# Kernel tuning notes

Measured on AMD Instinct MI355X. Metric: run time of the kernel, lower is better.

## Reference

```python
import jax, jax.numpy as jnp
import numpy as np

IN_C = 64
OUT_C = 128
HEADS = 8
DIM = 9 * IN_C  # 576


def unfold3x3_s2(fea):
    # torch.nn.functional.unfold(fea, (3,3), padding=1, stride=2)
    # returns [N, C*9, L] with channel-major (c, kh, kw) ordering.
    N, C, H, W = fea.shape
    Ho, Wo = H // 2, W // 2
    p = jnp.pad(fea, ((0, 0), (0, 0), (1, 1), (1, 1)))
    patches = jnp.stack(
        [p[:, :, ki:ki + 2 * Ho:2, kj:kj + 2 * Wo:2] for ki in range(3) for kj in range(3)],
        axis=2,
    )  # [N, C, 9, Ho, Wo]
    return patches.reshape(N, C * 9, Ho * Wo)


def mhsa(x, w_qkv, b_qkv, w_out, b_out):
    # standard ViT attention: x [B, L, D]
    B, L, D = x.shape
    dh = D // HEADS
    qkv = x @ w_qkv + b_qkv  # [B, L, 3D]
    q, k, v = jnp.split(qkv, 3, axis=-1)
    def heads(t):
        return t.reshape(B, L, HEADS, dh).transpose(0, 2, 1, 3)  # [B, h, L, dh]
    q, k, v = heads(q), heads(k), heads(v)
    scale = dh ** -0.5
    scores = jnp.einsum('bhqd,bhkd->bhqk', q, k) * scale
    attn = jax.nn.softmax(scores, axis=-1)
    o = jnp.einsum('bhqk,bhkd->bhqd', attn, v)  # [B, h, L, dh]
    o = o.transpose(0, 2, 1, 3).reshape(B, L, D)
    return o @ w_out + b_out


def setup_inputs() -> dict:
    key = jax.random.key(0)
    ks = jax.random.split(key, 6)
    s = DIM ** -0.5
    return {
        'fea': jax.random.normal(ks[0], (1, IN_C, 128, 128), dtype=jnp.float32),
        'w_qkv': jax.random.normal(ks[1], (DIM, 3 * DIM), dtype=jnp.float32) * s,
        'b_qkv': jnp.zeros((3 * DIM,), dtype=jnp.float32),
        'w_out': jax.random.normal(ks[2], (DIM, DIM), dtype=jnp.float32) * s,
        'b_out': jnp.zeros((DIM,), dtype=jnp.float32),
        'conv_w': jax.random.normal(ks[3], (OUT_C, IN_C, 3, 3), dtype=jnp.float32) * s,
    }


def reference(fea, w_qkv, b_qkv, w_out, b_out, conv_w):
    N, C, H, W = fea.shape
    Ho, Wo = H // 2, W // 2
    x = unfold3x3_s2(fea).transpose(0, 2, 1)          # [N, L, 9C]
    x = mhsa(x, w_qkv, b_qkv, w_out, b_out) + x       # residual
    # matmul with reshaped conv weights: [N, L, 9C] @ [9C, out_c]
    y = x @ conv_w.reshape(OUT_C, -1).T               # [N, L, out_c]
    y = y.transpose(0, 2, 1).reshape(N, OUT_C, Ho, Wo)  # fold with (1,1) kernel
    return jax.nn.silu(y)
```

## Files before the change

### kernel.cpp

```cpp
#include <hip/hip_runtime.h>
#include <hip/hip_bf16.h>
#include <math.h>

#define L_TOK 4096
#define D_DIM 576
#define NHEADS 8
#define DHEAD 72
#define DPAD 96
#define HSZ ((size_t)NHEADS * L_TOK * DPAD)
#define KSPLIT 4
#define LOG2E 1.4426950408889634f
#define SCALE2 (0.11785113019775792f * 1.4426950408889634f)

typedef __attribute__((ext_vector_type(8))) short short8;
typedef __attribute__((ext_vector_type(4))) short short4v;
typedef __attribute__((ext_vector_type(4))) float float4v;

union F4S8 {
  float4 f4;
  short8 s8;
  __hip_bfloat16 h[8];
};

__device__ inline void tc_body(const float* __restrict__ src,
                               __hip_bfloat16* __restrict__ dst, int R, int C,
                               int bi, int bj, int t, __hip_bfloat16* Ts) {
  const int col = t & 63, row4 = t >> 6;
#pragma unroll
  for (int u = 0; u < 16; u++) {
    int r = u * 4 + row4;
    Ts[r * 68 + col] = __float2bfloat16(src[(size_t)(bj * 64 + r) * C + bi * 64 + col]);
  }
  __syncthreads();
#pragma unroll
  for (int u = 0; u < 16; u++) {
    int c = u * 4 + row4;
    dst[(size_t)(bi * 64 + c) * R + bj * 64 + col] = Ts[col * 68 + c];
  }
}

__global__ __launch_bounds__(256) void prep_all(const float* __restrict__ fea,
                                                const float* __restrict__ w_qkv,
                                                const float* __restrict__ w_out,
                                                const float* __restrict__ conv_w,
                                                __hip_bfloat16* __restrict__ xb,
                                                __hip_bfloat16* __restrict__ WqkvT,
                                                __hip_bfloat16* __restrict__ WoT,
                                                __hip_bfloat16* __restrict__ CwB) {
  __shared__ float Shm[3120];
  const int b = blockIdx.x;
  const int t = threadIdx.x;
  if (b < 512) {
    float* Lf = Shm;
    const int ho = b & 63;
    const int c0 = (b >> 6) * 8;
    for (int e = t; e < 3072; e += 256) {
      int c = e / 384;
      int rr = (e / 128) % 3;
      int w = e & 127;
      int h = 2 * ho + rr - 1;
      float v = 0.f;
      if ((unsigned)h < 128u) v = fea[(size_t)(c0 + c) * 16384 + h * 128 + w];
      Lf[(c * 3 + rr) * 130 + w + 1] = v;
    }
    if (t < 24) { Lf[t * 130] = 0.f; Lf[t * 130 + 129] = 0.f; }
    __syncthreads();
    for (int e = t; e < 576; e += 256) {
      int wo = e / 9, ch = e - wo * 9;
      F4S8 u;
#pragma unroll
      for (int j = 0; j < 8; j++) {
        int dd = ch * 8 + j;
        int c = dd / 9, k = dd - c * 9;
        int ki = k / 3, kj = k - ki * 3;
        u.h[j] = __float2bfloat16(Lf[(c * 3 + ki) * 130 + 2 * wo + kj]);
      }
      *(float4*)(xb + (size_t)(ho * 64 + wo) * D_DIM + c0 * 9 + ch * 8) = u.f4;
    }
  } else if (b < 755) {
    int bb = b - 512;
    tc_body(w_qkv, WqkvT, D_DIM, 1728, bb % 27, bb / 27, t, (__hip_bfloat16*)Shm);
  } else if (b < 836) {
    int bb = b - 755;
    tc_body(w_out, WoT, D_DIM, D_DIM, bb % 9, bb / 9, t, (__hip_bfloat16*)Shm);
  } else {
    int i = (b - 836) * 256 + t;
    CwB[i] = __float2bfloat16(conv_w[i]);
  }
}

template <int EPI, int NMI>
__global__ __launch_bounds__(256) void gemm_mfma(const __hip_bfloat16* __restrict__ A,
                                                 const __hip_bfloat16* __restrict__ Bt,
                                                 const float* __restrict__ bias,
                                                 const __hip_bfloat16* __restrict__ resid,
                                                 __hip_bfloat16* __restrict__ outB,
                                                 __hip_bfloat16* __restrict__ outB2) {
  constexpr int K = D_DIM;
  constexpr int BM = NMI * 32;
  __shared__ __align__(16) __hip_bfloat16 As[BM * 72];
  __shared__ __align__(16) __hip_bfloat16 Bs[64 * 72];
  const int t = threadIdx.x;
  const int wave = t >> 6, lane = t & 63, quad = lane >> 4, l16 = lane & 15;
  const int wm = (wave & 2) * (NMI * 8);
  const int wn = (wave & 1) * 32;
  const int m0 = blockIdx.x * BM, n0 = blockIdx.y * 64;

  float4v acc[NMI][2];
#pragma unroll
  for (int i = 0; i < NMI; i++)
#pragma unroll
    for (int j = 0; j < 2; j++) acc[i][j] = (float4v){0.f, 0.f, 0.f, 0.f};

  const int arow = t >> 3, ach = t & 7;
  for (int k0 = 0; k0 < K; k0 += 64) {
    __syncthreads();
#pragma unroll
    for (int u = 0; u < NMI; u++) {
      int row = u * 32 + arow;
      *(float4*)(&As[row * 72 + ach * 8]) =
          *(const float4*)(A + (size_t)(m0 + row) * K + k0 + ach * 8);
    }
#pragma unroll
    for (int u = 0; u < 2; u++) {
      int row = u * 32 + arow;
      *(float4*)(&Bs[row * 72 + ach * 8]) =
          *(const float4*)(Bt + (size_t)(n0 + row) * K + k0 + ach * 8);
    }
    __syncthreads();
    short8 af[NMI][2], bfr[2][2];
#pragma unroll
    for (int i = 0; i < NMI; i++)
#pragma unroll
      for (int s = 0; s < 2; s++)
        af[i][s] = *(const short8*)(&As[(wm + i * 16 + l16) * 72 + s * 32 + quad * 8]);
#pragma unroll
    for (int j = 0; j < 2; j++)
#pragma unroll
      for (int s = 0; s < 2; s++)
        bfr[j][s] = *(const short8*)(&Bs[(wn + j * 16 + l16) * 72 + s * 32 + quad * 8]);
#pragma unroll
    for (int i = 0; i < NMI; i++)
#pragma unroll
      for (int j = 0; j < 2; j++) {
        acc[i][j] = __builtin_amdgcn_mfma_f32_16x16x32_bf16(af[i][0], bfr[j][0], acc[i][j], 0, 0, 0);
        acc[i][j] = __builtin_amdgcn_mfma_f32_16x16x32_bf16(af[i][1], bfr[j][1], acc[i][j], 0, 0, 0);
      }
  }

  if (EPI == 0) {
    const int part = n0 / D_DIM;
    if (part < 2) {
      __hip_bfloat16* dst = outB + (size_t)part * HSZ;
      const float sc = (part == 0) ? SCALE2 : 1.f;
#pragma unroll
      for (int j = 0; j < 2; j++) {
        int ng = n0 + wn + j * 16 + l16;
        float bv = bias[ng];
        int rem = ng - part * D_DIM;
        int h = rem / DHEAD;
        int d = rem - h * DHEAD;
#pragma unroll
        for (int i = 0; i < NMI; i++) {
          int mb = m0 + wm + i * 16 + quad * 4;
#pragma unroll
          for (int r = 0; r < 4; r++)
            dst[((size_t)h * L_TOK + mb + r) * DPAD + d] =
                __float2bfloat16((acc[i][j][r] + bv) * sc);
        }
      }
    } else {
      __hip_bfloat16* Ls = As;
      __syncthreads();
      const int n0rel = n0 - 2 * D_DIM;
#pragma unroll
      for (int j = 0; j < 2; j++) {
        int nloc = wn + j * 16 + l16;
        float bv = bias[n0 + nloc];
#pragma unroll
        for (int i = 0; i < NMI; i++) {
          int mloc = wm + i * 16 + quad * 4;
#pragma unroll
          for (int r = 0; r < 4; r++)
            Ls[nloc * 136 + mloc + r] = __float2bfloat16(acc[i][j][r] + bv);
        }
      }
      __syncthreads();
      for (int e = t; e < 1024; e += 256) {
        int row = e >> 4, ch = e & 15;
        int ng = n0rel + row;
        int hh = ng / DHEAD, dd = ng - hh * DHEAD;
        *(float4*)(outB2 + ((size_t)hh * DPAD + dd) * L_TOK + m0 + ch * 8) =
            *(const float4*)(&Ls[row * 136 + ch * 8]);
      }
    }
  } else {
#pragma unroll
    for (int j = 0; j < 2; j++) {
      int ng = n0 + wn + j * 16 + l16;
      float bv = bias[ng];
#pragma unroll
      for (int i = 0; i < NMI; i++) {
        int mb = m0 + wm + i * 16 + quad * 4;
#pragma unroll
        for (int r = 0; r < 4; r++) {
          size_t idx = (size_t)(mb + r) * D_DIM + ng;
          float v = acc[i][j][r] + bv + __bfloat162float(resid[idx]);
          outB[idx] = __float2bfloat16(v);
        }
      }
    }
  }
}

__global__ __launch_bounds__(256) void final_small(const __hip_bfloat16* __restrict__ A,
                                                   const __hip_bfloat16* __restrict__ Bt,
                                                   float* __restrict__ out) {
  __shared__ __align__(16) __hip_bfloat16 As[32 * 72];
  __shared__ __align__(16) __hip_bfloat16 Bs[32 * 72];
  const int t = threadIdx.x;
  const int wave = t >> 6, lane = t & 63, quad = lane >> 4, l16 = lane & 15;
  const int wm = (wave & 2) * 8;
  const int wn = (wave & 1) * 16;
  const int m0 = blockIdx.x * 32, n0 = blockIdx.y * 32;

  float4v acc = (float4v){0.f, 0.f, 0.f, 0.f};

  const int arow = t >> 3, ach = t & 7;
  for (int k0 = 0; k0 < D_DIM; k0 += 64) {
    __syncthreads();
    *(float4*)(&As[arow * 72 + ach * 8]) =
        *(const float4*)(A + (size_t)(m0 + arow) * D_DIM + k0 + ach * 8);
    *(float4*)(&Bs[arow * 72 + ach * 8]) =
        *(const float4*)(Bt + (size_t)(n0 + arow) * D_DIM + k0 + ach * 8);
    __syncthreads();
    short8 af[2], bfr[2];
#pragma unroll
    for (int s = 0; s < 2; s++) {
      af[s] = *(const short8*)(&As[(wm + l16) * 72 + s * 32 + quad * 8]);
      bfr[s] = *(const short8*)(&Bs[(wn + l16) * 72 + s * 32 + quad * 8]);
    }
    acc = __builtin_amdgcn_mfma_f32_16x16x32_bf16(af[0], bfr[0], acc, 0, 0, 0);
    acc = __builtin_amdgcn_mfma_f32_16x16x32_bf16(af[1], bfr[1], acc, 0, 0, 0);
  }
  const int oc = n0 + wn + l16;
  const int mb = m0 + wm + quad * 4;
#pragma unroll
  for (int r = 0; r < 4; r++) {
    float v = acc[r];
    float sg = 1.f / (1.f + __expf(-v));
    out[(size_t)oc * L_TOK + mb + r] = v * sg;
  }
}

#define KS_STRIDE 88
#define VT_STRIDE 72
#define PS_STRIDE 40
#define KBUF (64 * KS_STRIDE)
#define VBUF (74 * VT_STRIDE)

__global__ __launch_bounds__(256, 3) void attn_mfma(const __hip_bfloat16* __restrict__ Qb,
                                                    const __hip_bfloat16* __restrict__ Kb,
                                                    const __hip_bfloat16* __restrict__ VbT,
                                                    __hip_bfloat16* __restrict__ Opart,
                                                    float* __restrict__ Ml) {
  __shared__ __align__(16) __hip_bfloat16 Ks[2 * KBUF];
  __shared__ __align__(16) __hip_bfloat16 Vt[2 * VBUF];
  __shared__ __align__(16) __hip_bfloat16 Ps[4 * 32 * PS_STRIDE];

  const int bid = blockIdx.x;
  const int h = bid & 7;
  const int rest = bid >> 3;
  const int ksp = rest & 3;
  const int qblk = rest >> 2;
  const int t = threadIdx.x;
  const int wave = t >> 6;
  const int lane = t & 63;
  const int quad = lane >> 4;
  const int l16 = lane & 15;

  const __hip_bfloat16* Qh = Qb + (size_t)h * L_TOK * DPAD;
  const __hip_bfloat16* Kh = Kb + (size_t)h * L_TOK * DPAD;
  const __hip_bfloat16* VhT = VbT + (size_t)h * DPAD * L_TOK;

  const int qbase = qblk * 128 + wave * 32;
  short8 qf[2][3];
#pragma unroll
  for (int mi = 0; mi < 2; mi++) {
#pragma unroll
    for (int s = 0; s < 3; s++) {
      if (s == 2 && quad >= 1) {
        qf[mi][s] = (short8){0, 0, 0, 0, 0, 0, 0, 0};
        if (quad == 1) qf[mi][s][0] = (short)0xC100;
      } else {
        qf[mi][s] = *(const short8*)(Qh + (size_t)(qbase + mi * 16 + l16) * DPAD + s * 32 + quad * 8);
      }
    }
  }

  {
    const float4 zero4 = {0.f, 0.f, 0.f, 0.f};
    union { float4 f4; unsigned u[4]; } kpad, vones;
    kpad.u[0] = 0x00003F80u; kpad.u[1] = 0u; kpad.u[2] = 0u; kpad.u[3] = 0u;
    vones.u[0] = vones.u[1] = vones.u[2] = vones.u[3] = 0x3F803F80u;
    if (t < 128) {
      int row = t & 63, buf = t >> 6;
      __hip_bfloat16* B = Ks + buf * KBUF;
      *(float4*)(&B[row * KS_STRIDE + 72]) = kpad.f4;
      *(float4*)(&B[row * KS_STRIDE + 80]) = zero4;
    } else if (t < 160) {
      int e = t - 128;
      int buf = e >> 4, r2 = (e >> 3) & 1, ch = e & 7;
      __hip_bfloat16* B = Vt + buf * VBUF;
      *(float4*)(&B[(72 + r2) * VT_STRIDE + ch * 8]) = r2 ? zero4 : vones.f4;
    }
  }

  float4v Of[2][5];
#pragma unroll
  for (int mi = 0; mi < 2; mi++)
#pragma unroll
    for (int nt = 0; nt < 5; nt++) Of[mi][nt] = (float4v){0.f, 0.f, 0.f, 0.f};

  __hip_bfloat16* myPs = Ps + wave * 32 * PS_STRIDE;
  const int kstart = ksp * 1024;

  int kgo[3], klo[3], vgo[3], vlo[3];
#pragma unroll
  for (int u = 0; u < 3; u++) {
    int e = t + u * 256;
    int ee = (e < 576) ? e : 0;
    int row = ee / 9, ch = ee - row * 9;
    kgo[u] = row * (DPAD * 2) + ch * 16;
    klo[u] = row * (KS_STRIDE * 2) + ch * 16;
    int d = ee >> 3, c2 = ee & 7;
    vgo[u] = d * (L_TOK * 2) + c2 * 16;
    vlo[u] = d * (VT_STRIDE * 2) + c2 * 16;
  }
  const bool has3 = (t < 64);

  float4 krg0, krg1, krg2, vrg0, vrg1, vrg2;
  auto load_K = [&](int kbase) {
    const char* Kt_ = (const char*)(Kh + (size_t)kbase * DPAD);
    krg0 = *(const float4*)(Kt_ + kgo[0]);
    krg1 = *(const float4*)(Kt_ + kgo[1]);
    if (has3) krg2 = *(const float4*)(Kt_ + kgo[2]);
  };
  auto load_V = [&](int kbase) {
    const char* Vg_ = (const char*)(VhT + kbase);
    vrg0 = *(const float4*)(Vg_ + vgo[0]);
    vrg1 = *(const float4*)(Vg_ + vgo[1]);
    if (has3) vrg2 = *(const float4*)(Vg_ + vgo[2]);
  };
  auto stage_write = [&](__hip_bfloat16* Kw, __hip_bfloat16* Vw) {
    *(float4*)((char*)Kw + klo[0]) = krg0;
    *(float4*)((char*)Kw + klo[1]) = krg1;
    *(float4*)((char*)Vw + vlo[0]) = vrg0;
    *(float4*)((char*)Vw + vlo[1]) = vrg1;
    if (has3) {
      *(float4*)((char*)Kw + klo[2]) = krg2;
      *(float4*)((char*)Vw + vlo[2]) = vrg2;
    }
  };

  auto body = [&](int kt, const __hip_bfloat16* Ksb, const __hip_bfloat16* Vtb,
                  __hip_bfloat16* Kw, __hip_bfloat16* Vw) {
    const int knext = (kt < 15) ? kt + 1 : 15;
    load_K(kstart + knext * 64);

    float4v S[2][4];
    __builtin_amdgcn_s_setprio(1);
#pragma unroll
    for (int ks = 0; ks < 4; ks++) {
      float4v a0 = (float4v){0.f, 0.f, 0.f, 0.f};
      float4v a1 = a0;
#pragma unroll
      for (int s = 0; s < 2; s++) {
        short8 kf = *(const short8*)(&Ksb[(ks * 16 + l16) * KS_STRIDE + s * 32 + quad * 8]);
        a0 = __builtin_amdgcn_mfma_f32_16x16x32_bf16(kf, qf[0][s], a0, 0, 0, 0);
        a1 = __builtin_amdgcn_mfma_f32_16x16x32_bf16(kf, qf[1][s], a1, 0, 0, 0);
      }
      {
        int c2s = 64 + (quad < 2 ? quad * 8 : 16);
        short8 kf2 = *(const short8*)(&Ksb[(ks * 16 + l16) * KS_STRIDE + c2s]);
        a0 = __builtin_amdgcn_mfma_f32_16x16x32_bf16(kf2, qf[0][2], a0, 0, 0, 0);
        a1 = __builtin_amdgcn_mfma_f32_16x16x32_bf16(kf2, qf[1][2], a1, 0, 0, 0);
      }
#pragma unroll
      for (int r = 0; r < 4; r++) { S[0][ks][r] = a0[r]; S[1][ks][r] = a1[r]; }
    }
    __builtin_amdgcn_s_setprio(0);

    load_V(kstart + knext * 64);

#pragma unroll
    for (int kstep = 0; kstep < 2; kstep++) {
#pragma unroll
      for (int mi = 0; mi < 2; mi++) {
#pragma unroll
        for (int k2 = 0; k2 < 2; k2++) {
          int ks = kstep * 2 + k2;
          union { short4v v; __hip_bfloat16 hh[4]; } pk;
#pragma unroll
          for (int r = 0; r < 4; r++)
            pk.hh[r] = __float2bfloat16(exp2f(S[mi][ks][r]));
          *(short4v*)(&myPs[(mi * 16 + l16) * PS_STRIDE + k2 * 16 + quad * 4]) = pk.v;
        }
      }
      short8 pa[2];
#pragma unroll
      for (int mi = 0; mi < 2; mi++)
        pa[mi] = *(const short8*)(&myPs[(mi * 16 + l16) * PS_STRIDE + quad * 8]);
      __builtin_amdgcn_s_setprio(1);
#pragma unroll
      for (int nt = 0; nt < 4; nt++) {
        short8 vb = *(const short8*)(&Vtb[(nt * 16 + l16) * VT_STRIDE + kstep * 32 + quad * 8]);
        Of[0][nt] = __builtin_amdgcn_mfma_f32_16x16x32_bf16(pa[0], vb, Of[0][nt], 0, 0, 0);
        Of[1][nt] = __builtin_amdgcn_mfma_f32_16x16x32_bf16(pa[1], vb, Of[1][nt], 0, 0, 0);
      }
      {
        int vrow = 64 + l16;
        vrow = vrow > 73 ? 73 : vrow;
        short8 vb4 = *(const short8*)(&Vtb[vrow * VT_STRIDE + kstep * 32 + quad * 8]);
        Of[0][4] = __builtin_amdgcn_mfma_f32_16x16x32_bf16(pa[0], vb4, Of[0][4], 0, 0, 0);
        Of[1][4] = __builtin_amdgcn_mfma_f32_16x16x32_bf16(pa[1], vb4, Of[1][4], 0, 0, 0);
      }
      __builtin_amdgcn_s_setprio(0);
    }

    stage_write(Kw, Vw);
    __syncthreads();
  };

  load_K(kstart);
  load_V(kstart);
  stage_write(Ks, Vt);
  __syncthreads();

  for (int kt2 = 0; kt2 < 16; kt2 += 2) {
    body(kt2,     Ks,        Vt,        Ks + KBUF, Vt + VBUF);
    body(kt2 + 1, Ks + KBUF, Vt + VBUF, Ks,        Vt);
  }

  const size_t pb = ((size_t)ksp * NHEADS + h) * L_TOK;
#pragma unroll
  for (int mi = 0; mi < 2; mi++) {
#pragma unroll
    for (int nt = 0; nt < 5; nt++) {
      int d = nt * 16 + l16;
      if (d < DHEAD) {
#pragma unroll
        for (int r = 0; r < 4; r++) {
          int q = qbase + mi * 16 + quad * 4 + r;
          Opart[(pb + q) * 72 + d] = __float2bfloat16(Of[mi][nt][r]);
        }
      }
    }
  }
  if (l16 == 8) {
#pragma unroll
    for (int mi = 0; mi < 2; mi++) {
#pragma unroll
      for (int r = 0; r < 4; r++)
        Ml[pb + qbase + mi * 16 + quad * 4 + r] = Of[mi][4][r];
    }
  }
}

__global__ __launch_bounds__(256) void attn_merge(const __hip_bfloat16* __restrict__ Opart,
                                                  const float* __restrict__ Ml,
                                                  __hip_bfloat16* __restrict__ ob) {
  int idx = blockIdx.x * 256 + threadIdx.x;
  int h = idx / (L_TOK * 9);
  int rem = idx - h * (L_TOK * 9);
  int q = rem / 9;
  int ch = rem - q * 9;
  float denom = 0.f;
  float acc[8] = {0, 0, 0, 0, 0, 0, 0, 0};
#pragma unroll
  for (int s = 0; s < KSPLIT; s++) {
    size_t b = ((size_t)s * NHEADS + h) * L_TOK + q;
    denom += Ml[b];
    short8 o = *(const short8*)(Opart + b * 72 + ch * 8);
#pragma unroll
    for (int j = 0; j < 8; j++) {
      union { short ss; __hip_bfloat16 bb; } u;
      u.ss = o[j];
      acc[j] += __bfloat162float(u.bb);
    }
  }
  float inv = 1.f / denom;
  __hip_bfloat16* dst = ob + (size_t)q * D_DIM + h * DHEAD + ch * 8;
#pragma unroll
  for (int j = 0; j < 8; j++) dst[j] = __float2bfloat16(acc[j] * inv);
}

extern "C" void kernel_launch(void* const* d_in, const int* in_sizes, int n_in,
                              void* d_out, int out_size, void* d_ws, size_t ws_size,
                              hipStream_t stream) {
  const float* fea    = (const float*)d_in[0];
  const float* w_qkv  = (const float*)d_in[1];
  const float* b_qkv  = (const float*)d_in[2];
  const float* w_out  = (const float*)d_in[3];
  const float* b_out  = (const float*)d_in[4];
  const float* conv_w = (const float*)d_in[5];
  float* out = (float*)d_out;

  __hip_bfloat16* xb    = (__hip_bfloat16*)d_ws;
  __hip_bfloat16* WqkvT = xb + (size_t)L_TOK * D_DIM;
  __hip_bfloat16* WoT   = WqkvT + (size_t)1728 * D_DIM;
  __hip_bfloat16* CwB   = WoT + (size_t)D_DIM * D_DIM;
  __hip_bfloat16* QKb   = CwB + (size_t)128 * D_DIM;
  __hip_bfloat16* VbT   = QKb + 2 * HSZ;
  __hip_bfloat16* Opart = VbT + HSZ;
  float* Ml = (float*)(Opart + (size_t)KSPLIT * NHEADS * L_TOK * 72);
  __hip_bfloat16* ob = QKb;
  __hip_bfloat16* xr = Opart;

  prep_all<<<1124, 256, 0, stream>>>(fea, w_qkv, w_out, conv_w, xb, WqkvT, WoT, CwB);
  gemm_mfma<0, 4><<<dim3(32, 27), 256, 0, stream>>>(xb, WqkvT, b_qkv, nullptr, QKb, VbT);
  attn_mfma<<<1024, 256, 0, stream>>>(QKb, QKb + HSZ, VbT, Opart, Ml);
  attn_merge<<<1152, 256, 0, stream>>>(Opart, Ml, ob);
  gemm_mfma<1, 2><<<dim3(64, 9), 256, 0, stream>>>(ob, WoT, b_out, xb, xr, nullptr);
  final_small<<<dim3(128, 4), 256, 0, stream>>>(xr, CwB, out);
}
```

Measured before the change: 179.1 us.

## Stage K/V tiles with direct global-to-LDS loads and XOR-swizzled V layout

Replaces register-staged K/V tile loads (global to VGPR, then LDS store) with global_load_lds 16-byte direct copies into packed, unpadded LDS tiles. V columns are XOR-swizzled on the global side so packed rows avoid bank conflicts. The padding rows and columns now come from a small constant LDS array selected per lane. This removes register pressure and extra LDS store instructions, at the cost of relying on correct vmcnt handling across the barrier and of per-lane pointer selects for the pad fragments.

Result: faster. 173.2 us (-3.3%).

```diff
diff --git a/kernel.cpp b/kernel.cpp
--- a/kernel.cpp
+++ b/kernel.cpp
@@ -21,6 +21,12 @@
   short8 s8;
   __hip_bfloat16 h[8];
 };
+
+__device__ __forceinline__ void gl16(const void* g, void* l) {
+  __builtin_amdgcn_global_load_lds(
+      (const __attribute__((address_space(1))) unsigned int*)g,
+      (__attribute__((address_space(3))) unsigned int*)l, 16, 0, 0);
+}
 
 __device__ inline void tc_body(const float* __restrict__ src,
                                __hip_bfloat16* __restrict__ dst, int R, int C,
@@ -253,20 +259,21 @@
   }
 }
 
-#define KS_STRIDE 88
-#define VT_STRIDE 72
+#define KSE 72
+#define VSE 64
+#define KTILE (64 * KSE)
+#define VTILE (72 * VSE)
 #define PS_STRIDE 40
-#define KBUF (64 * KS_STRIDE)
-#define VBUF (74 * VT_STRIDE)
 
 __global__ __launch_bounds__(256, 3) void attn_mfma(const __hip_bfloat16* __restrict__ Qb,
                                                     const __hip_bfloat16* __restrict__ Kb,
                                                     const __hip_bfloat16* __restrict__ VbT,
                                                     __hip_bfloat16* __restrict__ Opart,
                                                     float* __restrict__ Ml) {
-  __shared__ __align__(16) __hip_bfloat16 Ks[2 * KBUF];
-  __shared__ __align__(16) __hip_bfloat16 Vt[2 * VBUF];
+  __shared__ __align__(16) __hip_bfloat16 Ks[2 * KTILE];
+  __shared__ __align__(16) __hip_bfloat16 Vt[2 * VTILE];
   __shared__ __align__(16) __hip_bfloat16 Ps[4 * 32 * PS_STRIDE];
+  __shared__ __align__(16) __hip_bfloat16 PadC[32];
 
   const int bid = blockIdx.x;
   const int h = bid & 7;
@@ -283,6 +290,14 @@
   const __hip_bfloat16* Kh = Kb + (size_t)h * L_TOK * DPAD;
   const __hip_bfloat16* VhT = VbT + (size_t)h * DPAD * L_TOK;
 
+  if (t < 4) {
+    union { float4 f4; unsigned u[4]; } pv;
+    pv.u[0] = pv.u[1] = pv.u[2] = pv.u[3] = 0u;
+    if (t == 0) pv.u[0] = 0x00003F80u;
+    if (t == 2) pv.u[0] = pv.u[1] = pv.u[2] = pv.u[3] = 0x3F803F80u;
+    *(float4*)(&PadC[t * 8]) = pv.f4;
+  }
+
   const int qbase = qblk * 128 + wave * 32;
   short8 qf[2][3];
 #pragma unroll
@@ -298,24 +313,6 @@
     }
   }
 
-  {
-    const float4 zero4 = {0.f, 0.f, 0.f, 0.f};
-    union { float4 f4; unsigned u[4]; } kpad, vones;
-    kpad.u[0] = 0x00003F80u; kpad.u[1] = 0u; kpad.u[2] = 0u; kpad.u[3] = 0u;
-    vones.u[0] = vones.u[1] = vones.u[2] = vones.u[3] = 0x3F803F80u;
-    if (t < 128) {
-      int row = t & 63, buf = t >> 6;
-      __hip_bfloat16* B = Ks + buf * KBUF;
-      *(float4*)(&B[row * KS_STRIDE + 72]) = kpad.f4;
-      *(float4*)(&B[row * KS_STRIDE + 80]) = zero4;
-    } else if (t < 160) {
-      int e = t - 128;
-      int buf = e >> 4, r2 = (e >> 3) & 1, ch = e & 7;
-      __hip_bfloat16* B = Vt + buf * VBUF;
-      *(float4*)(&B[(72 + r2) * VT_STRIDE + ch * 8]) = r2 ? zero4 : vones.f4;
-    }
-  }
-
   float4v Of[2][5];
 #pragma unroll
   for (int mi = 0; mi < 2; mi++)
@@ -325,49 +322,35 @@
   __hip_bfloat16* myPs = Ps + wave * 32 * PS_STRIDE;
   const int kstart = ksp * 1024;
 
-  int kgo[3], klo[3], vgo[3], vlo[3];
+  int kgo[3], vgo[3];
 #pragma unroll
   for (int u = 0; u < 3; u++) {
     int e = t + u * 256;
     int ee = (e < 576) ? e : 0;
     int row = ee / 9, ch = ee - row * 9;
     kgo[u] = row * (DPAD * 2) + ch * 16;
-    klo[u] = row * (KS_STRIDE * 2) + ch * 16;
     int d = ee >> 3, c2 = ee & 7;
-    vgo[u] = d * (L_TOK * 2) + c2 * 16;
-    vlo[u] = d * (VT_STRIDE * 2) + c2 * 16;
-  }
-  const bool has3 = (t < 64);
-
-  float4 krg0, krg1, krg2, vrg0, vrg1, vrg2;
-  auto load_K = [&](int kbase) {
-    const char* Kt_ = (const char*)(Kh + (size_t)kbase * DPAD);
-    krg0 = *(const float4*)(Kt_ + kgo[0]);
-    krg1 = *(const float4*)(Kt_ + kgo[1]);
-    if (has3) krg2 = *(const float4*)(Kt_ + kgo[2]);
+    vgo[u] = d * (L_TOK * 2) + ((c2 ^ (d & 7)) * 16);
+  }
+
+  auto stage = [&](int kbase, int p) {
+    const char* Kg = (const char*)(Kh + (size_t)kbase * DPAD);
+    const char* Vg = (const char*)(VhT + kbase);
+    char* Kl = (char*)Ks + p * (KTILE * 2) + t * 16;
+    char* Vl = (char*)Vt + p * (VTILE * 2) + t * 16;
+    gl16(Kg + kgo[0], Kl);
+    gl16(Kg + kgo[1], Kl + 4096);
+    gl16(Vg + vgo[0], Vl);
+    gl16(Vg + vgo[1], Vl + 4096);
+    if (wave == 0) {
+      gl16(Kg + kgo[2], Kl + 8192);
+      gl16(Vg + vgo[2], Vl + 8192);
+    }
   };
-  auto load_V = [&](int kbase) {
-    const char* Vg_ = (const char*)(VhT + kbase);
-    vrg0 = *(const float4*)(Vg_ + vgo[0]);
-    vrg1 = *(const float4*)(Vg_ + vgo[1]);
-    if (has3) vrg2 = *(const float4*)(Vg_ + vgo[2]);
-  };
-  auto stage_write = [&](__hip_bfloat16* Kw, __hip_bfloat16* Vw) {
-    *(float4*)((char*)Kw + klo[0]) = krg0;
-    *(float4*)((char*)Kw + klo[1]) = krg1;
-    *(float4*)((char*)Vw + vlo[0]) = vrg0;
-    *(float4*)((char*)Vw + vlo[1]) = vrg1;
-    if (has3) {
-      *(float4*)((char*)Kw + klo[2]) = krg2;
-      *(float4*)((char*)Vw + vlo[2]) = vrg2;
-    }
-  };
-
-  auto body = [&](int kt, const __hip_bfloat16* Ksb, const __hip_bfloat16* Vtb,
-                  __hip_bfloat16* Kw, __hip_bfloat16* Vw) {
-    const int knext = (kt < 15) ? kt + 1 : 15;
-    load_K(kstart + knext * 64);
-
+
+  const int vswz = l16 & 7;
+
+  auto compute = [&](const __hip_bfloat16* Ksb, const __hip_bfloat16* Vtb) {
     float4v S[2][4];
     __builtin_amdgcn_s_setprio(1);
 #pragma unroll
@@ -376,13 +359,15 @@
       float4v a1 = a0;
 #pragma unroll
       for (int s = 0; s < 2; s++) {
-        short8 kf = *(const short8*)(&Ksb[(ks * 16 + l16) * KS_STRIDE + s * 32 + quad * 8]);
+        short8 kf = *(const short8*)(&Ksb[(ks * 16 + l16) * KSE + s * 32 + quad * 8]);
         a0 = __builtin_amdgcn_mfma_f32_16x16x32_bf16(kf, qf[0][s], a0, 0, 0, 0);
         a1 = __builtin_amdgcn_mfma_f32_16x16x32_bf16(kf, qf[1][s], a1, 0, 0, 0);
       }
       {
-        int c2s = 64 + (quad < 2 ? quad * 8 : 16);
-        short8 kf2 = *(const short8*)(&Ksb[(ks * 16 + l16) * KS_STRIDE + c2s]);
+        const __hip_bfloat16* areal = &Ksb[(ks * 16 + l16) * KSE + 64];
+        const __hip_bfloat16* apad = &PadC[(quad >= 2) ? 8 : 0];
+        const __hip_bfloat16* ap = (quad == 0) ? areal : apad;
+        short8 kf2 = *(const short8*)ap;
         a0 = __builtin_amdgcn_mfma_f32_16x16x32_bf16(kf2, qf[0][2], a0, 0, 0, 0);
         a1 = __builtin_amdgcn_mfma_f32_16x16x32_bf16(kf2, qf[1][2], a1, 0, 0, 0);
       }
@@ -390,8 +375,6 @@
       for (int r = 0; r < 4; r++) { S[0][ks][r] = a0[r]; S[1][ks][r] = a1[r]; }
     }
     __builtin_amdgcn_s_setprio(0);
-
-    load_V(kstart + knext * 64);
 
 #pragma unroll
     for (int kstep = 0; kstep < 2; kstep++) {
@@ -412,34 +395,35 @@
       for (int mi = 0; mi < 2; mi++)
         pa[mi] = *(const short8*)(&myPs[(mi * 16 + l16) * PS_STRIDE + quad * 8]);
       __builtin_amdgcn_s_setprio(1);
+      const int csw = ((kstep * 4 + quad) ^ vswz) * 8;
 #pragma unroll
       for (int nt = 0; nt < 4; nt++) {
-        short8 vb = *(const short8*)(&Vtb[(nt * 16 + l16) * VT_STRIDE + kstep * 32 + quad * 8]);
+        short8 vb = *(const short8*)(&Vtb[(nt * 16 + l16) * VSE + csw]);
         Of[0][nt] = __builtin_amdgcn_mfma_f32_16x16x32_bf16(pa[0], vb, Of[0][nt], 0, 0, 0);
         Of[1][nt] = __builtin_amdgcn_mfma_f32_16x16x32_bf16(pa[1], vb, Of[1][nt], 0, 0, 0);
       }
       {
-        int vrow = 64 + l16;
-        vrow = vrow > 73 ? 73 : vrow;
-        short8 vb4 = *(const short8*)(&Vtb[vrow * VT_STRIDE + kstep * 32 + quad * 8]);
+        const __hip_bfloat16* areal = &Vtb[(64 + l16) * VSE + csw];
+        const __hip_bfloat16* apad = &PadC[16 + ((l16 == 8) ? 0 : 8)];
+        const __hip_bfloat16* ap = (l16 < 8) ? areal : apad;
+        short8 vb4 = *(const short8*)ap;
         Of[0][4] = __builtin_amdgcn_mfma_f32_16x16x32_bf16(pa[0], vb4, Of[0][4], 0, 0, 0);
         Of[1][4] = __builtin_amdgcn_mfma_f32_16x16x32_bf16(pa[1], vb4, Of[1][4], 0, 0, 0);
       }
       __builtin_amdgcn_s_setprio(0);
     }
-
-    stage_write(Kw, Vw);
-    __syncthreads();
   };
 
-  load_K(kstart);
-  load_V(kstart);
-  stage_write(Ks, Vt);
+  stage(kstart, 0);
   __syncthreads();
 
   for (int kt2 = 0; kt2 < 16; kt2 += 2) {
-    body(kt2,     Ks,        Vt,        Ks + KBUF, Vt + VBUF);
-    body(kt2 + 1, Ks + KBUF, Vt + VBUF, Ks,        Vt);
+    if (kt2 + 1 < 16) stage(kstart + (kt2 + 1) * 64, 1);
+    compute(Ks, Vt);
+    __syncthreads();
+    if (kt2 + 2 < 16) stage(kstart + (kt2 + 2) * 64, 0);
+    compute(Ks + KTILE, Vt + VTILE);
+    __syncthreads();
   }
 
   const size_t pb = ((size_t)ksp * NHEADS + h) * L_TOK;
```
